# Kernel optimization log

Measured on AMD Instinct MI355X. Metric: run time of the kernel, lower is better.

Reference implementation:

```python
import jax, jax.numpy as jnp
import numpy as np

H = 16  # num_heads


def setup_inputs() -> dict:
    key = jax.random.key(0)
    ks = jax.random.split(key, 12)
    b, n, c, T = 4, 1024, 512, 4096

    def lin_w(k, out_d, in_d):
        return jax.random.normal(k, (out_d, in_d), jnp.float32) * (1.0 / np.sqrt(in_d))

    return {
        "feat": jax.random.normal(ks[0], (b, n, c), jnp.float32),
        "member_idx": jax.random.randint(ks[1], (b, n), 0, n),
        "cluster_mask": jnp.ones((b, n), jnp.int32),
        "pe_idx": jax.random.randint(ks[2], (b, n, n), 0, T),
        "global_attn": 1,
        "pre_table": jax.random.normal(ks[3], (T, 5), jnp.float32),
        "q_w": lin_w(ks[4], c, c), "q_b": jnp.zeros((c,), jnp.float32),
        "kv_w": lin_w(ks[5], 2 * c, c), "kv_b": jnp.zeros((2 * c,), jnp.float32),
        "pe_w": lin_w(ks[6], H, 5), "pe_b": jnp.zeros((H,), jnp.float32),
        "blank_k": jax.random.normal(ks[7], (c,), jnp.float32) * 0.2,
        "blank_v": jax.random.normal(ks[8], (c,), jnp.float32) * 0.2,
        "proj_w": lin_w(ks[9], c, c), "proj_b": jnp.zeros((c,), jnp.float32),
    }


def reference(feat, member_idx, cluster_mask, pe_idx, global_attn, pre_table,
              q_w, q_b, kv_w, kv_b, pe_w, pe_b, blank_k, blank_v, proj_w, proj_b):
    # global_attn path only (member_idx / cluster_mask unused in this branch)
    b, n, c = feat.shape
    h = H
    c_ = c // h
    scale = c_ ** -0.5

    q = (feat @ q_w.T + q_b) * scale                      # [b,n,c]
    q = q.reshape(b, n, h, c_).transpose(0, 2, 1, 3)      # [b,h,n,c_]
    kv = (feat @ kv_w.T + kv_b).reshape(b, n, h, 2, c_)
    key = kv[..., 0, :].transpose(0, 2, 1, 3)             # [b,h,n,c_]
    v = kv[..., 1, :].transpose(0, 2, 1, 3)               # [b,h,n,c_]

    attn = jnp.einsum('bhqd,bhkd->bhqk', q, key)          # [b,h,n,n]

    pe_out = pre_table @ pe_w.T + pe_b                    # [T,h]
    pos = pe_out[pe_idx].transpose(0, 3, 1, 2)            # [b,h,n,n]
    attn = attn + pos

    blank = jnp.sum(q * blank_k.reshape(1, h, 1, c_), axis=-1, keepdims=True)  # [b,h,n,1]
    attn = jax.nn.softmax(jnp.concatenate([attn, blank], axis=-1), axis=-1)
    blank_attn = attn[..., -1:]                           # [b,h,n,1]
    attn = attn[..., :-1]                                 # [b,h,n,n]

    out = jnp.einsum('bhqk,bhkd->bhqd', attn, v)          # [b,h,n,c_]
    out = out + blank_attn * blank_v.reshape(1, h, 1, c_)
    out = out.transpose(0, 2, 1, 3).reshape(b, n, c)
    return out @ proj_w.T + proj_b
```

## Files before the change

kernel.cpp:

```cpp
#include <hip/hip_runtime.h>
#include <hip/hip_fp16.h>

typedef __attribute__((ext_vector_type(8))) short short8;
typedef __attribute__((ext_vector_type(8))) __bf16 bf16x8;
typedef __attribute__((ext_vector_type(4))) float f32x4;
typedef __attribute__((ext_vector_type(16))) float f32x16;

#define DEV __device__ __forceinline__

DEV unsigned short f2bf(float f) {
    unsigned int u = __float_as_uint(f);
    return (unsigned short)((u + 0x7FFFu + ((u >> 16) & 1u)) >> 16);
}
DEV float bf2f(unsigned short s) { return __uint_as_float(((unsigned int)s) << 16); }
DEV bf16x8 asbf(short8 v) { return __builtin_bit_cast(bf16x8, v); }

DEV void gload16(const void* g, void* l) {
    __builtin_amdgcn_global_load_lds(
        (const __attribute__((address_space(1))) unsigned int*)g,
        (__attribute__((address_space(3))) unsigned int*)l, 16, 0, 0);
}

__global__ __launch_bounds__(256) void k_prep(const float* __restrict__ feat,
                                              const float* __restrict__ qw, const float* __restrict__ qb,
                                              const float* __restrict__ kvw, const float* __restrict__ kvb,
                                              const float* __restrict__ pew, const float* __restrict__ peb,
                                              const float* __restrict__ pret, const float* __restrict__ projw,
                                              unsigned short* __restrict__ featb,
                                              unsigned short* __restrict__ wqkv, float* __restrict__ bqkv,
                                              unsigned short* __restrict__ projwb, unsigned short* __restrict__ peG2) {
    const float scale = 0.17677669529663687f;
    int i0 = blockIdx.x * 256 + threadIdx.x;
    if (i0 < 262144) {
        const float4* f4 = (const float4*)feat + (size_t)i0 * 2;
        float4 a = f4[0], c = f4[1];
        short8 o;
        o[0] = (short)f2bf(a.x); o[1] = (short)f2bf(a.y);
        o[2] = (short)f2bf(a.z); o[3] = (short)f2bf(a.w);
        o[4] = (short)f2bf(c.x); o[5] = (short)f2bf(c.y);
        o[6] = (short)f2bf(c.z); o[7] = (short)f2bf(c.w);
        ((short8*)featb)[i0] = o;
        return;
    }
    int i = i0 - 262144;
    if (i < 786432) {
        int o = i >> 9, k = i & 511;
        float v = (o < 512) ? qw[(o << 9) + k] * scale : kvw[((o - 512) << 9) + k];
        wqkv[i] = f2bf(v);
    } else if (i < 786432 + 262144) {
        int j = i - 786432;
        projwb[j] = f2bf(projw[j]);
    } else if (i < 786432 + 262144 + 1536) {
        int o = i - (786432 + 262144);
        bqkv[o] = (o < 512) ? qb[o] * scale : kvb[o - 512];
    } else if (i < 786432 + 262144 + 1536 + 65536) {
        int j = i - (786432 + 262144 + 1536);
        int t = j >> 4, h = j & 15;
        float s = peb[h];
#pragma unroll
        for (int u = 0; u < 5; u++) s += pret[t * 5 + u] * pew[h * 5 + u];
        peG2[(size_t)(h >> 1) * 8192 + t * 2 + (h & 1)] =
            __builtin_bit_cast(unsigned short, __float2half(s));
    }
}

__global__ __launch_bounds__(256) void k_qkv(const unsigned short* __restrict__ A,
                                             const unsigned short* __restrict__ Bw,
                                             const float* __restrict__ bias,
                                             unsigned short* __restrict__ Qf,
                                             unsigned short* __restrict__ Kf,
                                             unsigned short* __restrict__ Vf) {
    __shared__ __align__(16) unsigned short As[128 * 64];
    __shared__ __align__(16) unsigned short Bs[64 * 64];
    int tid = threadIdx.x, lane = tid & 63, wid = tid >> 6;
    int m0 = blockIdx.y * 128, n0 = blockIdx.x * 64;
    int wm = wid >> 1, wn = wid & 1;
    int lr = lane >> 3, lk = (lane & 7) * 8;
    f32x4 acc[4][2] = {};

    for (int k0 = 0; k0 < 512; k0 += 64) {
#pragma unroll
        for (int i = 0; i < 4; i++) {
            int ch = wid * 4 + i;
            gload16(A + (size_t)(m0 + ch * 8 + lr) * 512 + k0 + lk, As + ch * 512);
        }
#pragma unroll
        for (int i = 0; i < 2; i++) {
            int ch = wid * 2 + i;
            gload16(Bw + (size_t)(n0 + ch * 8 + lr) * 512 + k0 + lk, Bs + ch * 512);
        }
        __syncthreads();
#pragma unroll
        for (int kk = 0; kk < 64; kk += 32) {
            short8 a[4], b[2];
#pragma unroll
            for (int m = 0; m < 4; m++)
                a[m] = *(const short8*)(As + (wm * 64 + m * 16 + (lane & 15)) * 64 + kk + ((lane >> 4) << 3));
#pragma unroll
            for (int n = 0; n < 2; n++)
                b[n] = *(const short8*)(Bs + (wn * 32 + n * 16 + (lane & 15)) * 64 + kk + ((lane >> 4) << 3));
#pragma unroll
            for (int m = 0; m < 4; m++) {
#pragma unroll
                for (int n = 0; n < 2; n++)
                    acc[m][n] = __builtin_amdgcn_mfma_f32_16x16x32_bf16(asbf(a[m]), asbf(b[n]), acc[m][n], 0, 0, 0);
            }
        }
        __syncthreads();
    }
#pragma unroll
    for (int m = 0; m < 4; m++) {
#pragma unroll
        for (int n = 0; n < 2; n++) {
            int col = n0 + wn * 32 + n * 16 + (lane & 15);
            float bv = bias[col];
#pragma unroll
            for (int r = 0; r < 4; r++) {
                int row = m0 + wm * 64 + m * 16 + ((lane >> 4) << 2) + r;
                float v = acc[m][n][r] + bv;
                unsigned short bb = f2bf(v);
                int batch = row >> 10, nn = row & 1023;
                if (col < 512) {
                    int h = col >> 5, d = col & 31;
                    int bh = (batch << 4) + h;
                    int qt = nn >> 5, q5 = nn & 31;
                    int sub = d >> 4, hi2 = (d >> 3) & 1, j = d & 7;
                    Qf[((((size_t)(bh * 32 + qt) * 2 + sub) * 64) + hi2 * 32 + q5) * 8 + j] = bb;
                } else {
                    int oo = col - 512, h = oo >> 6, rem = oo & 63;
                    int bh = (batch << 4) + h;
                    int kt = nn >> 6, ks = (nn >> 5) & 1;
                    if (rem < 32) {
                        int d = rem, half = d >> 4, hi2 = (d >> 3) & 1, j = d & 7, q5 = nn & 31;
                        Kf[((((size_t)((bh * 16 + kt) * 2 + ks) * 2 + half) * 64) + hi2 * 32 + q5) * 8 + j] = bb;
                    } else {
                        int d = rem - 32, nb = nn & 31;
                        int half = nb >> 4, hi2 = (nb >> 3) & 1, j = nb & 7;
                        Vf[((((size_t)((bh * 16 + kt) * 2 + ks) * 2 + half) * 64) + hi2 * 32 + d) * 8 + j] = bb;
                    }
                }
            }
        }
    }
}

__global__ __launch_bounds__(256, 4) void k_attn(const unsigned short* __restrict__ Qf,
                                                 const unsigned short* __restrict__ Kf,
                                                 const unsigned short* __restrict__ Vf,
                                                 const int* __restrict__ pe_idx,
                                                 const unsigned* __restrict__ peG2,
                                                 const float* __restrict__ blank_k,
                                                 const float* __restrict__ blank_v,
                                                 unsigned short* __restrict__ attnO) {
    __shared__ unsigned peT2[4096];
    __shared__ unsigned posS[128 * 33];

    int tid = threadIdx.x, lane = tid & 63, w = tid >> 6;
    int q5 = lane & 31, hi = lane >> 5;
    int bid = blockIdx.x;
    int b = bid & 3, qt = (bid >> 2) & 31, hg = (bid >> 7) & 7;
    int q0 = qt * 32;
    int hl = w & 1, khalf = w >> 1;
    int head = hg * 2 + hl, bh = (b << 4) + head;

    {
        const unsigned* pg = peG2 + (size_t)hg * 4096;
#pragma unroll
        for (int j2 = 0; j2 < 16; j2++) {
            int r = tid + 256 * j2;
            peT2[r] = pg[r];
        }
    }

    int sq = tid >> 3, kg = tid & 7;
    const int* pibase = pe_idx + ((size_t)((b << 10) + q0 + sq)) * 1024;

    short8 qf[2];
    float lb_, m_run, l_run;
    f32x16 accO = {};
    const f32x16 zero16 = {};

    {
        const unsigned short* qb_ = Qf + ((size_t)(bh * 32 + qt) * 2) * 512 + lane * 8;
        qf[0] = *(const short8*)(qb_);
        qf[1] = *(const short8*)(qb_ + 512);
        float dot = 0.f;
#pragma unroll
        for (int sub = 0; sub < 2; sub++) {
            const float* bk = blank_k + head * 32 + sub * 16 + hi * 8;
#pragma unroll
            for (int t = 0; t < 8; t++) dot += bf2f((unsigned short)qf[sub][t]) * bk[t];
        }
        dot += __shfl_xor(dot, 32, 64);
        lb_ = dot;
        m_run = (khalf == 0) ? dot : -1e30f;
        l_run = (khalf == 0) ? 1.0f : 0.0f;
    }

    int4 id4[4];
#pragma unroll
    for (int s = 0; s < 4; s++) {
        int col = (s < 2) ? (kg * 4 + 32 * s) : (512 + kg * 4 + 32 * (s - 2));
        id4[s] = *(const int4*)(pibase + col);
    }
    __syncthreads();

    for (int step = 0; step < 8; step++) {
#pragma unroll
        for (int s = 0; s < 4; s++) {
            int kb = kg * 4 + 32 * s;
            int id_[4] = {id4[s].x, id4[s].y, id4[s].z, id4[s].w};
#pragma unroll
            for (int c = 0; c < 4; c++)
                posS[(kb + c) * 33 + sq] = peT2[id_[c]];
        }
        __syncthreads();

        if (step < 7) {
#pragma unroll
            for (int s = 0; s < 4; s++) {
                int col = (s < 2) ? ((step + 1) * 64 + kg * 4 + 32 * s)
                                  : (512 + (step + 1) * 64 + kg * 4 + 32 * (s - 2));
                id4[s] = *(const int4*)(pibase + col);
            }
        }

        int ktg = khalf * 8 + step;
        f32x16 st[2];
#pragma unroll
        for (int ks = 0; ks < 2; ks++) {
            const unsigned short* kp = Kf + ((size_t)((bh * 16 + ktg) * 2 + ks) * 2) * 512 + lane * 8;
            short8 kf0 = *(const short8*)(kp);
            short8 kf1 = *(const short8*)(kp + 512);
            st[ks] = __builtin_amdgcn_mfma_f32_32x32x16_bf16(asbf(kf0), asbf(qf[0]), zero16, 0, 0, 0);
            st[ks] = __builtin_amdgcn_mfma_f32_32x32x16_bf16(asbf(kf1), asbf(qf[1]), st[ks], 0, 0, 0);
        }
#pragma unroll
        for (int ks = 0; ks < 2; ks++) {
#pragma unroll
            for (int r = 0; r < 16; r++) {
                int kl = (r & 3) + 8 * (r >> 2) + 4 * hi + 32 * ks;
                unsigned pd = posS[(khalf * 64 + kl) * 33 + q5];
                __half2 h2 = __builtin_bit_cast(__half2, pd);
                st[ks][r] += hl ? __high2float(h2) : __low2float(h2);
            }
        }
        float tm[16];
#pragma unroll
        for (int i = 0; i < 16; i++) tm[i] = fmaxf(st[0][i], st[1][i]);
#pragma unroll
        for (int i = 0; i < 8; i++) tm[i] = fmaxf(tm[i], tm[i + 8]);
#pragma unroll
        for (int i = 0; i < 4; i++) tm[i] = fmaxf(tm[i], tm[i + 4]);
        float mx = fmaxf(fmaxf(tm[0], tm[1]), fmaxf(tm[2], tm[3]));
        mx = fmaxf(mx, __shfl_xor(mx, 32, 64));
        if (!__all(mx <= m_run + 8.0f)) {
            float mn = fmaxf(m_run, mx);
            float fac = __expf(m_run - mn);
            m_run = mn;
            l_run *= fac;
#pragma unroll
            for (int r = 0; r < 16; r++) {
                int qrow = (r & 3) + 8 * (r >> 2) + 4 * hi;
                float facr = __shfl(fac, qrow, 64);
                accO[r] *= facr;
            }
        }
#pragma unroll
        for (int ks = 0; ks < 2; ks++)
#pragma unroll
            for (int r = 0; r < 16; r++)
                st[ks][r] = __expf(st[ks][r] - m_run);
        float ts[16];
#pragma unroll
        for (int i = 0; i < 16; i++) ts[i] = st[0][i] + st[1][i];
#pragma unroll
        for (int i = 0; i < 8; i++) ts[i] += ts[i + 8];
#pragma unroll
        for (int i = 0; i < 4; i++) ts[i] += ts[i + 4];
        float sum = (ts[0] + ts[1]) + (ts[2] + ts[3]);
        sum += __shfl_xor(sum, 32, 64);
        l_run += sum;
#pragma unroll
        for (int ks = 0; ks < 2; ks++) {
            unsigned pk_[8];
#pragma unroll
            for (int i = 0; i < 8; i++) {
                float plo = st[ks][2 * i], phi = st[ks][2 * i + 1];
                asm("v_cvt_pk_bf16_f32 %0, %1, %2" : "=v"(pk_[i]) : "v"(plo), "v"(phi));
            }
            asm("v_permlane32_swap_b32 %0, %1" : "+v"(pk_[0]), "+v"(pk_[2]));
            asm("v_permlane32_swap_b32 %0, %1" : "+v"(pk_[1]), "+v"(pk_[3]));
            asm("v_permlane32_swap_b32 %0, %1" : "+v"(pk_[4]), "+v"(pk_[6]));
            asm("v_permlane32_swap_b32 %0, %1" : "+v"(pk_[5]), "+v"(pk_[7]));
            uint4 u0 = {pk_[0], pk_[1], pk_[2], pk_[3]};
            uint4 u1 = {pk_[4], pk_[5], pk_[6], pk_[7]};
            short8 pa0 = __builtin_bit_cast(short8, u0);
            short8 pa1 = __builtin_bit_cast(short8, u1);
            const unsigned short* vp = Vf + ((size_t)((bh * 16 + ktg) * 2 + ks) * 2) * 512 + lane * 8;
            short8 vf0 = *(const short8*)(vp);
            short8 vf1 = *(const short8*)(vp + 512);
            accO = __builtin_amdgcn_mfma_f32_32x32x16_bf16(asbf(pa0), asbf(vf0), accO, 0, 0, 0);
            accO = __builtin_amdgcn_mfma_f32_32x32x16_bf16(asbf(pa1), asbf(vf1), accO, 0, 0, 0);
        }
        __syncthreads();
    }

    float* fb = (float*)posS;
    float* mS = fb + 2176;
    float* lS = mS + 64;
    if (khalf == 1) {
#pragma unroll
        for (int r = 0; r < 16; r++)
            fb[(hl * 64 + lane) * 17 + r] = accO[r];
        if (hi == 0) {
            mS[hl * 32 + q5] = m_run;
            lS[hl * 32 + q5] = l_run;
        }
    }
    __syncthreads();
    if (khalf == 0) {
        float mB = mS[hl * 32 + q5], lB = lS[hl * 32 + q5];
        float M = fmaxf(m_run, mB);
        float eA = __expf(m_run - M), eB = __expf(mB - M);
        float L = l_run * eA + lB * eB;
        float inv = 1.0f / L;
        float bw = __expf(lb_ - M) * inv;
        float bv = blank_v[head * 32 + q5];
#pragma unroll
        for (int r = 0; r < 16; r++) {
            int qrow = (r & 3) + 8 * (r >> 2) + 4 * hi;
            float eA_r = __shfl(eA, qrow, 64);
            float eB_r = __shfl(eB, qrow, 64);
            float inv_r = __shfl(inv, qrow, 64);
            float bw_r = __shfl(bw, qrow, 64);
            float accB = fb[(hl * 64 + lane) * 17 + r];
            float ov = (accO[r] * eA_r + accB * eB_r) * inv_r + bw_r * bv;
            attnO[((size_t)((b << 10) + q0 + qrow)) * 512 + head * 32 + q5] = f2bf(ov);
        }
    }
}

__global__ __launch_bounds__(256) void k_proj(const unsigned short* __restrict__ A,
                                              const unsigned short* __restrict__ Bw,
                                              const float* __restrict__ bias,
                                              float* __restrict__ out) {
    __shared__ __align__(16) unsigned short As[128 * 64];
    __shared__ __align__(16) unsigned short Bs[64 * 64];
    int tid = threadIdx.x, lane = tid & 63, wid = tid >> 6;
    int m0 = blockIdx.y * 128, n0 = blockIdx.x * 64;
    int wm = wid >> 1, wn = wid & 1;
    int lr = lane >> 3, lk = (lane & 7) * 8;
    f32x4 acc[4][2] = {};

    for (int k0 = 0; k0 < 512; k0 += 64) {
#pragma unroll
        for (int i = 0; i < 4; i++) {
            int ch = wid * 4 + i;
            gload16(A + (size_t)(m0 + ch * 8 + lr) * 512 + k0 + lk, As + ch * 512);
        }
#pragma unroll
        for (int i = 0; i < 2; i++) {
            int ch = wid * 2 + i;
            gload16(Bw + (size_t)(n0 + ch * 8 + lr) * 512 + k0 + lk, Bs + ch * 512);
        }
        __syncthreads();
#pragma unroll
        for (int kk = 0; kk < 64; kk += 32) {
            short8 a[4], b[2];
#pragma unroll
            for (int m = 0; m < 4; m++)
                a[m] = *(const short8*)(As + (wm * 64 + m * 16 + (lane & 15)) * 64 + kk + ((lane >> 4) << 3));
#pragma unroll
            for (int n = 0; n < 2; n++)
                b[n] = *(const short8*)(Bs + (wn * 32 + n * 16 + (lane & 15)) * 64 + kk + ((lane >> 4) << 3));
#pragma unroll
            for (int m = 0; m < 4; m++) {
#pragma unroll
                for (int n = 0; n < 2; n++)
                    acc[m][n] = __builtin_amdgcn_mfma_f32_16x16x32_bf16(asbf(a[m]), asbf(b[n]), acc[m][n], 0, 0, 0);
            }
        }
        __syncthreads();
    }
#pragma unroll
    for (int m = 0; m < 4; m++) {
#pragma unroll
        for (int n = 0; n < 2; n++) {
            int col = n0 + wn * 32 + n * 16 + (lane & 15);
            float bv = bias[col];
#pragma unroll
            for (int r = 0; r < 4; r++) {
                int row = m0 + wm * 64 + m * 16 + ((lane >> 4) << 2) + r;
                out[(size_t)row * 512 + col] = acc[m][n][r] + bv;
            }
        }
    }
}

extern "C" void kernel_launch(void* const* d_in, const int* in_sizes, int n_in,
                              void* d_out, int out_size, void* d_ws, size_t ws_size,
                              hipStream_t stream) {
    const float* feat    = (const float*)d_in[0];
    const int*   pe_idx  = (const int*)d_in[3];
    const float* pret    = (const float*)d_in[5];
    const float* qw      = (const float*)d_in[6];
    const float* qb      = (const float*)d_in[7];
    const float* kvw     = (const float*)d_in[8];
    const float* kvb     = (const float*)d_in[9];
    const float* pew     = (const float*)d_in[10];
    const float* peb     = (const float*)d_in[11];
    const float* blank_k = (const float*)d_in[12];
    const float* blank_v = (const float*)d_in[13];
    const float* projw   = (const float*)d_in[14];
    const float* projb   = (const float*)d_in[15];

    char* ws = (char*)d_ws;
    unsigned short* featb  = (unsigned short*)(ws);
    unsigned short* wqkv   = (unsigned short*)(ws + 4194304);
    unsigned short* projwb = (unsigned short*)(ws + 5767168);
    float*          bqkv   = (float*)(ws + 6291456);
    unsigned short* peG2   = (unsigned short*)(ws + 6297600);
    unsigned short* Qf     = (unsigned short*)(ws + 6428672);
    unsigned short* Kf     = (unsigned short*)(ws + 10622976);
    unsigned short* Vf     = (unsigned short*)(ws + 14817280);
    unsigned short* attnO  = featb;

    k_prep<<<dim3(5382), dim3(256), 0, stream>>>(feat, qw, qb, kvw, kvb, pew, peb, pret, projw,
                                                 featb, wqkv, bqkv, projwb, peG2);
    k_qkv<<<dim3(24, 32), dim3(256), 0, stream>>>(featb, wqkv, bqkv, Qf, Kf, Vf);
    k_attn<<<dim3(1024), dim3(256), 0, stream>>>(Qf, Kf, Vf, pe_idx, (const unsigned*)peG2,
                                                 blank_k, blank_v, attnO);
    k_proj<<<dim3(8, 32), dim3(256), 0, stream>>>(attnO, projwb, projb, (float*)d_out);
}
```

Before: 72.75 us.

## Swizzle GEMM LDS tiles, vectorize pos-bias LDS layout, raise MFMA priority

The QKV and projection GEMMs now XOR-swizzle the 16-byte chunk index when staging A/B tiles into LDS and when reading them back, to avoid bank conflicts on the short8 fragment reads. In the attention kernel the gathered position-bias buffer is transposed to a query-major layout with a stride of 132, so writes and reads use 128-bit LDS accesses instead of scalar ones. s_setprio is also raised around the MFMA blocks to favour matrix issue. The swizzle must match exactly between the global_load_lds writes and the fragment reads. The new position layout reuses the same buffer for the final reduction scratch.

After: 70.20 us. 3.5% less time.

```diff
diff --git a/kernel.cpp b/kernel.cpp
--- a/kernel.cpp
+++ b/kernel.cpp
@@ -75,7 +75,9 @@
     int tid = threadIdx.x, lane = tid & 63, wid = tid >> 6;
     int m0 = blockIdx.y * 128, n0 = blockIdx.x * 64;
     int wm = wid >> 1, wn = wid & 1;
-    int lr = lane >> 3, lk = (lane & 7) * 8;
+    int q16 = lane & 15, g = lane >> 4;
+    int lr = lane >> 3;
+    int lk = ((lane & 7) ^ lr) * 8;
     f32x4 acc[4][2] = {};
 
     for (int k0 = 0; k0 < 512; k0 += 64) {
@@ -92,13 +94,18 @@
         __syncthreads();
 #pragma unroll
         for (int kk = 0; kk < 64; kk += 32) {
+            int c8 = (kk >> 3) + g;
             short8 a[4], b[2];
 #pragma unroll
-            for (int m = 0; m < 4; m++)
-                a[m] = *(const short8*)(As + (wm * 64 + m * 16 + (lane & 15)) * 64 + kk + ((lane >> 4) << 3));
-#pragma unroll
-            for (int n = 0; n < 2; n++)
-                b[n] = *(const short8*)(Bs + (wn * 32 + n * 16 + (lane & 15)) * 64 + kk + ((lane >> 4) << 3));
+            for (int m = 0; m < 4; m++) {
+                int row = wm * 64 + m * 16 + q16;
+                a[m] = *(const short8*)(As + row * 64 + ((c8 ^ (q16 & 7)) << 3));
+            }
+#pragma unroll
+            for (int n = 0; n < 2; n++) {
+                int row = wn * 32 + n * 16 + q16;
+                b[n] = *(const short8*)(Bs + row * 64 + ((c8 ^ (q16 & 7)) << 3));
+            }
 #pragma unroll
             for (int m = 0; m < 4; m++) {
 #pragma unroll
@@ -112,11 +119,11 @@
     for (int m = 0; m < 4; m++) {
 #pragma unroll
         for (int n = 0; n < 2; n++) {
-            int col = n0 + wn * 32 + n * 16 + (lane & 15);
+            int col = n0 + wn * 32 + n * 16 + q16;
             float bv = bias[col];
 #pragma unroll
             for (int r = 0; r < 4; r++) {
-                int row = m0 + wm * 64 + m * 16 + ((lane >> 4) << 2) + r;
+                int row = m0 + wm * 64 + m * 16 + (g << 2) + r;
                 float v = acc[m][n][r] + bv;
                 unsigned short bb = f2bf(v);
                 int batch = row >> 10, nn = row & 1023;
@@ -153,7 +160,7 @@
                                                  const float* __restrict__ blank_v,
                                                  unsigned short* __restrict__ attnO) {
     __shared__ unsigned peT2[4096];
-    __shared__ unsigned posS[128 * 33];
+    __shared__ __align__(16) unsigned posS2[32 * 132];
 
     int tid = threadIdx.x, lane = tid & 63, w = tid >> 6;
     int q5 = lane & 31, hi = lane >> 5;
@@ -208,11 +215,10 @@
     for (int step = 0; step < 8; step++) {
 #pragma unroll
         for (int s = 0; s < 4; s++) {
-            int kb = kg * 4 + 32 * s;
-            int id_[4] = {id4[s].x, id4[s].y, id4[s].z, id4[s].w};
-#pragma unroll
-            for (int c = 0; c < 4; c++)
-                posS[(kb + c) * 33 + sq] = peT2[id_[c]];
+            uint4 wv;
+            wv.x = peT2[id4[s].x]; wv.y = peT2[id4[s].y];
+            wv.z = peT2[id4[s].z]; wv.w = peT2[id4[s].w];
+            *(uint4*)&posS2[sq * 132 + kg * 4 + 32 * s] = wv;
         }
         __syncthreads();
 
@@ -227,6 +233,7 @@
 
         int ktg = khalf * 8 + step;
         f32x16 st[2];
+        __builtin_amdgcn_s_setprio(1);
 #pragma unroll
         for (int ks = 0; ks < 2; ks++) {
             const unsigned short* kp = Kf + ((size_t)((bh * 16 + ktg) * 2 + ks) * 2) * 512 + lane * 8;
@@ -235,14 +242,18 @@
             st[ks] = __builtin_amdgcn_mfma_f32_32x32x16_bf16(asbf(kf0), asbf(qf[0]), zero16, 0, 0, 0);
             st[ks] = __builtin_amdgcn_mfma_f32_32x32x16_bf16(asbf(kf1), asbf(qf[1]), st[ks], 0, 0, 0);
         }
+        __builtin_amdgcn_s_setprio(0);
 #pragma unroll
         for (int ks = 0; ks < 2; ks++) {
 #pragma unroll
-            for (int r = 0; r < 16; r++) {
-                int kl = (r & 3) + 8 * (r >> 2) + 4 * hi + 32 * ks;
-                unsigned pd = posS[(khalf * 64 + kl) * 33 + q5];
-                __half2 h2 = __builtin_bit_cast(__half2, pd);
-                st[ks][r] += hl ? __high2float(h2) : __low2float(h2);
+            for (int rr = 0; rr < 4; rr++) {
+                uint4 v = *(const uint4*)&posS2[q5 * 132 + khalf * 64 + rr * 8 + 4 * hi + 32 * ks];
+                unsigned pv[4] = {v.x, v.y, v.z, v.w};
+#pragma unroll
+                for (int c = 0; c < 4; c++) {
+                    __half2 h2 = __builtin_bit_cast(__half2, pv[c]);
+                    st[ks][rr * 4 + c] += hl ? __high2float(h2) : __low2float(h2);
+                }
             }
         }
         float tm[16];
@@ -300,13 +311,15 @@
             const unsigned short* vp = Vf + ((size_t)((bh * 16 + ktg) * 2 + ks) * 2) * 512 + lane * 8;
             short8 vf0 = *(const short8*)(vp);
             short8 vf1 = *(const short8*)(vp + 512);
+            __builtin_amdgcn_s_setprio(1);
             accO = __builtin_amdgcn_mfma_f32_32x32x16_bf16(asbf(pa0), asbf(vf0), accO, 0, 0, 0);
             accO = __builtin_amdgcn_mfma_f32_32x32x16_bf16(asbf(pa1), asbf(vf1), accO, 0, 0, 0);
-        }
-        __syncthreads();
-    }
-
-    float* fb = (float*)posS;
+            __builtin_amdgcn_s_setprio(0);
+        }
+        __syncthreads();
+    }
+
+    float* fb = (float*)posS2;
     float* mS = fb + 2176;
     float* lS = mS + 64;
     if (khalf == 1) {
@@ -350,7 +363,9 @@
     int tid = threadIdx.x, lane = tid & 63, wid = tid >> 6;
     int m0 = blockIdx.y * 128, n0 = blockIdx.x * 64;
     int wm = wid >> 1, wn = wid & 1;
-    int lr = lane >> 3, lk = (lane & 7) * 8;
+    int q16 = lane & 15, g = lane >> 4;
+    int lr = lane >> 3;
+    int lk = ((lane & 7) ^ lr) * 8;
     f32x4 acc[4][2] = {};
 
     for (int k0 = 0; k0 < 512; k0 += 64) {
@@ -367,13 +382,18 @@
         __syncthreads();
 #pragma unroll
         for (int kk = 0; kk < 64; kk += 32) {
+            int c8 = (kk >> 3) + g;
             short8 a[4], b[2];
 #pragma unroll
-            for (int m = 0; m < 4; m++)
-                a[m] = *(const short8*)(As + (wm * 64 + m * 16 + (lane & 15)) * 64 + kk + ((lane >> 4) << 3));
-#pragma unroll
-            for (int n = 0; n < 2; n++)
-                b[n] = *(const short8*)(Bs + (wn * 32 + n * 16 + (lane & 15)) * 64 + kk + ((lane >> 4) << 3));
+            for (int m = 0; m < 4; m++) {
+                int row = wm * 64 + m * 16 + q16;
+                a[m] = *(const short8*)(As + row * 64 + ((c8 ^ (q16 & 7)) << 3));
+            }
+#pragma unroll
+            for (int n = 0; n < 2; n++) {
+                int row = wn * 32 + n * 16 + q16;
+                b[n] = *(const short8*)(Bs + row * 64 + ((c8 ^ (q16 & 7)) << 3));
+            }
 #pragma unroll
             for (int m = 0; m < 4; m++) {
 #pragma unroll
@@ -387,11 +407,11 @@
     for (int m = 0; m < 4; m++) {
 #pragma unroll
         for (int n = 0; n < 2; n++) {
-            int col = n0 + wn * 32 + n * 16 + (lane & 15);
+            int col = n0 + wn * 32 + n * 16 + q16;
             float bv = bias[col];
 #pragma unroll
             for (int r = 0; r < 4; r++) {
-                int row = m0 + wm * 64 + m * 16 + ((lane >> 4) << 2) + r;
+                int row = m0 + wm * 64 + m * 16 + (g << 2) + r;
                 out[(size_t)row * 512 + col] = acc[m][n][r] + bv;
             }
         }
```
